# Kernel tuning notes

Measured on AMD Instinct MI355X. Metric: run time of the kernel, lower is better.

The kernel has to match this reference:

```python
import jax, jax.numpy as jnp
import numpy as np

K_TOP = 8
TEMP = 1.0
GUMBEL_EPS = 1e-20
GEN_EPS = 1e-7
NEG_INF = -1e9


def _genconv(xn, src, dst, e, We, be, W1, b1, W2, b2):
    """GENConv: edge-proj, m=relu(x_src+e)+eps, per-dst softmax aggregation (t=1),
    residual add, then 2-layer MLP."""
    N = xn.shape[0]
    ep = e @ We + be                         # [E, C]
    m = jax.nn.relu(xn[src] + ep) + GEN_EPS  # [E, C]
    mx = jax.ops.segment_max(m, dst, num_segments=N)
    mx = jnp.where(jnp.isfinite(mx), mx, 0.0)
    w = jnp.exp(m - mx[dst])
    den = jax.ops.segment_sum(w, dst, num_segments=N)
    agg = jax.ops.segment_sum(w * m, dst, num_segments=N) / jnp.where(den > 0, den, 1.0)
    out = agg + xn
    return jax.nn.relu(out @ W1 + b1) @ W2 + b2


def setup_inputs() -> dict:
    key = jax.random.key(0)
    ks = jax.random.split(key, 16)
    N, E, D, ED = 1024, 16384, 128, 16
    H1, H2, OUT = 64, 64, 40
    s = 0.02
    return {
        "x": jax.random.normal(ks[0], (N, D), jnp.float32),
        "edge_attr": jax.random.normal(ks[1], (E, ED), jnp.float32),
        "gumbel_u": jax.random.uniform(ks[2], (N, N), jnp.float32),
        "mlp_w": jax.random.normal(ks[3], (ED + 2 * D, 1), jnp.float32) * s,
        "mlp_b": jnp.zeros((1,), jnp.float32),
        "c1_we": jax.random.normal(ks[4], (ED, D), jnp.float32) * s,
        "c1_be": jnp.zeros((D,), jnp.float32),
        "c1_w1": jax.random.normal(ks[5], (D, 2 * D), jnp.float32) * s,
        "c1_b1": jnp.zeros((2 * D,), jnp.float32),
        "c1_w2": jax.random.normal(ks[6], (2 * D, H1), jnp.float32) * s,
        "c1_b2": jnp.zeros((H1,), jnp.float32),
        "c2_we": jax.random.normal(ks[7], (ED, H1), jnp.float32) * s,
        "c2_be": jnp.zeros((H1,), jnp.float32),
        "c2_w1": jax.random.normal(ks[8], (H1, 2 * H1), jnp.float32) * s,
        "c2_b1": jnp.zeros((2 * H1,), jnp.float32),
        "c2_w2": jax.random.normal(ks[9], (2 * H1, H2), jnp.float32) * s,
        "c2_b2": jnp.zeros((H2,), jnp.float32),
        "fc_w": jax.random.normal(ks[10], (H2, OUT), jnp.float32) * s,
        "fc_b": jnp.zeros((OUT,), jnp.float32),
        "num_nodes": N,
        "edge_index": jax.random.randint(ks[11], (2, E), 0, N),
        "node_mask": jnp.ones((N,), jnp.int32),
    }


def reference(x, edge_attr, gumbel_u, mlp_w, mlp_b,
              c1_we, c1_be, c1_w1, c1_b1, c1_w2, c1_b2,
              c2_we, c2_be, c2_w1, c2_b1, c2_w2, c2_b2,
              fc_w, fc_b, num_nodes, edge_index, node_mask):
    N, D = x.shape
    src, dst = edge_index[0], edge_index[1]

    # dense adjacency (duplicate edges sum, only used as a zero/nonzero mask)
    adj = jnp.zeros((N, N), x.dtype).at[src, dst].add(1.0)

    # Edge-score MLP on concat([x_u, x_v*mask, edge_attr_dense]) decomposed
    # linearly (same math as scoring the dense [N,N,2D+ED] feature tensor).
    w_node, w_nb, w_e = mlp_w[:D], mlp_w[D:2 * D], mlp_w[2 * D:]
    s_edge = jnp.zeros((N, N), x.dtype).at[src, dst].set((edge_attr @ w_e)[:, 0])
    score = (x @ w_node) + (x @ w_nb).T * (adj > 0) + s_edge + mlp_b[0]
    score = jnp.where(adj == 0, NEG_INF, score)

    z = jax.nn.softmax(score, axis=-1)
    g = -jnp.log(-jnp.log(gumbel_u + GUMBEL_EPS) + GUMBEL_EPS)
    z = jax.nn.softmax((z + g) / TEMP, axis=-1)

    # top-k edge sampling; softmax output is strictly positive so valid_mask
    # (z>0) is always all-True and shapes stay static at N*k edges.
    _, topi = jax.lax.top_k(z, K_TOP)                       # [N, k]
    new_src = jnp.repeat(jnp.arange(N), K_TOP)
    new_dst = topi.reshape(-1)

    # match each new edge against old edge list (argmax of boolean equality,
    # unmatched edges fall back to index 0 exactly as torch argmax does)
    eq = (edge_index[0][None, :] == new_src[:, None]) & \
         (edge_index[1][None, :] == new_dst[:, None])       # [N*k, E]
    new_attr = edge_attr[jnp.argmax(eq, axis=-1)]

    h = _genconv(x, new_src, new_dst, new_attr, c1_we, c1_be, c1_w1, c1_b1, c1_w2, c1_b2)
    h = jax.nn.relu(h)
    h = _genconv(h, new_src, new_dst, new_attr, c2_we, c2_be, c2_w1, c2_b1, c2_w2, c2_b2)
    h = jax.nn.relu(h)
    out = h @ fc_w + fc_b
    # node_mask is all ones, so x[node_mask != 0] == identity; masked write
    # keeps static shapes under jit.
    return jnp.where((node_mask != 0)[:, None], out, 0.0)
```

## Files before the change

kernel.cpp:

```cpp
#include <hip/hip_runtime.h>
#include <cfloat>

#define NN   1024
#define NE   16384
#define D0   128
#define EDIM 16
#define NH1  64
#define NOUT 40
#define KTOP 8
#define NEGINF (-1000000000.0f)
#define MAXDEG 64
#define PMAX   64

#define OFF_EM  0u
#define OFF_ND  32768u
#define OFF_H   65536u

__device__ __forceinline__ void amx(float& v, int& j, float ov, int oj) {
    if (ov > v || (ov == v && oj < j)) { v = ov; j = oj; }
}

__global__ __launch_bounds__(256) void topk_kernel(
    const float* __restrict__ x, const float* __restrict__ ea,
    const float* __restrict__ u, const float* __restrict__ mlp_w,
    const float* __restrict__ mlp_b, const int* __restrict__ ei,
    int* __restrict__ nd, int* __restrict__ em)
{
    __shared__ int idmx[4 * NN];
    __shared__ int idmn[4 * NN];
    __shared__ int plj[4 * PMAX];
    __shared__ int ple[4 * PMAX];
    __shared__ int np[4];
    const int t = threadIdx.x, lane = t & 63, w = t >> 6;
    const int r0 = blockIdx.x * 4;

    #pragma unroll
    for (int q = 0; q < 16; q++) { idmx[t + q * 256] = -1; idmn[t + q * 256] = 0x7FFFFFFF; }
    if (t < 4) np[t] = 0;
    __syncthreads();

    const int4* src4 = (const int4*)ei;
    #pragma unroll
    for (int q = 0; q < 16; q++) {
        int idx4 = t + q * 256;
        int4 v = src4[idx4];
        int e0 = idx4 * 4;
        #pragma unroll
        for (int c = 0; c < 4; c++) {
            int s = (c == 0) ? v.x : (c == 1) ? v.y : (c == 2) ? v.z : v.w;
            unsigned rr = (unsigned)(s - r0);
            if (rr < 4u) {
                int e = e0 + c;
                int d = ei[NE + e];
                atomicMax(&idmx[rr * NN + d], e);
                atomicMin(&idmn[rr * NN + d], e);
            }
        }
    }
    __syncthreads();

    #pragma unroll
    for (int q = 0; q < 16; q++) {
        int idx = t + q * 256;
        int e = idmx[idx];
        if (e >= 0) {
            int row = idx >> 10;
            int p = atomicAdd(&np[row], 1);
            if (p < PMAX) { plj[row * PMAX + p] = idx & 1023; ple[row * PMAX + p] = e; }
        }
    }
    __syncthreads();

    const int r = r0 + w;

    float part = x[r * D0 + lane] * mlp_w[lane] + x[r * D0 + 64 + lane] * mlp_w[64 + lane];
    for (int s2 = 32; s2; s2 >>= 1) part += __shfl_down(part, s2);
    const float arb = __shfl(part, 0) + mlp_b[0];

    float val[16];
    #pragma unroll
    for (int q = 0; q < 16; q++) val[q] = NEGINF;

    const int npw = min(np[w], PMAX);
    for (int p = 0; p < npw; p++) {
        int j = plj[w * PMAX + p], e = ple[w * PMAX + p];
        float pp = x[j * D0 + lane] * mlp_w[128 + lane]
                 + x[j * D0 + 64 + lane] * mlp_w[192 + lane];
        if (lane < 16) pp += ea[e * EDIM + lane] * mlp_w[256 + lane];
        for (int s2 = 32; s2; s2 >>= 1) pp += __shfl_down(pp, s2);
        float sc = __shfl(pp, 0) + arb;
        #pragma unroll
        for (int q = 0; q < 16; q++)
            if (q == (j >> 6) && lane == (j & 63)) val[q] = sc;
    }

    float lm = NEGINF;
    #pragma unroll
    for (int q = 0; q < 16; q++) lm = fmaxf(lm, val[q]);
    for (int s2 = 32; s2; s2 >>= 1) lm = fmaxf(lm, __shfl_down(lm, s2));
    const float rowmax = __shfl(lm, 0);
    const bool noedge = (rowmax == NEGINF);

    float ls = 0.f;
    #pragma unroll
    for (int q = 0; q < 16; q++) {
        float ev = noedge ? 1.0f : ((val[q] == NEGINF) ? 0.0f : expf(val[q] - rowmax));
        val[q] = ev; ls += ev;
    }
    for (int s2 = 32; s2; s2 >>= 1) ls += __shfl_down(ls, s2);
    const float rsum = __shfl(ls, 0);

    const float* ur = u + r * NN;
    #pragma unroll
    for (int q = 0; q < 16; q++) {
        float uu = ur[q * 64 + lane];
        float g = -logf(-logf(uu + 1e-20f) + 1e-20f);
        val[q] = val[q] / rsum + g;
    }

    for (int sel = 0; sel < KTOP; sel++) {
        float bv = -FLT_MAX; int bj = NN;
        #pragma unroll
        for (int q = 0; q < 16; q++) amx(bv, bj, val[q], q * 64 + lane);
        for (int s2 = 32; s2; s2 >>= 1) {
            float ov = __shfl_down(bv, s2); int oj = __shfl_down(bj, s2);
            amx(bv, bj, ov, oj);
        }
        int wj = __shfl(bj, 0);
        if (lane == 0) {
            int mn = idmn[w * NN + wj];
            em[r * KTOP + sel] = (mn == 0x7FFFFFFF) ? 0 : mn;
            nd[r * KTOP + sel] = wj;
        }
        #pragma unroll
        for (int q = 0; q < 16; q++)
            if (q == (wj >> 6) && lane == (wj & 63)) val[q] = -FLT_MAX;
    }
}

__global__ __launch_bounds__(256) void genconv1_kernel(
    const float* __restrict__ x, const float* __restrict__ ea,
    const float* __restrict__ we_g, const float* __restrict__ be,
    const float* __restrict__ w1, const float* __restrict__ b1,
    const float* __restrict__ w2, const float* __restrict__ b2,
    const int* __restrict__ nd, const int* __restrict__ em,
    float* __restrict__ h)
{
    __shared__ int   slots[2][MAXDEG];
    __shared__ float eatt[2][MAXDEG * EDIM];
    __shared__ float arow[2][D0];
    __shared__ float t1s[2][2 * D0];
    __shared__ int   cnts[2];
    const int t = threadIdx.x, sub = t >> 7, d = t & 127;
    const int r0 = blockIdx.x * 2;
    const int r = r0 + sub;
    if (t < 2) cnts[t] = 0;
    __syncthreads();

    const int4* nd4 = (const int4*)nd;
    #pragma unroll
    for (int q = 0; q < 8; q++) {
        int idx4 = t + q * 256;
        int4 v = nd4[idx4];
        int n0 = idx4 * 4;
        #pragma unroll
        for (int c = 0; c < 4; c++) {
            int dj = (c == 0) ? v.x : (c == 1) ? v.y : (c == 2) ? v.z : v.w;
            unsigned rr = (unsigned)(dj - r0);
            if (rr < 2u) {
                int p = atomicAdd(&cnts[rr], 1);
                if (p < MAXDEG) slots[rr][p] = n0 + c;
            }
        }
    }
    __syncthreads();
    const int cnt = min(cnts[sub], MAXDEG);
    if (d == 0) {
        for (int p = 1; p < cnt; p++) {
            int v = slots[sub][p]; int q = p - 1;
            while (q >= 0 && slots[sub][q] > v) { slots[sub][q + 1] = slots[sub][q]; q--; }
            slots[sub][q + 1] = v;
        }
    }
    __syncthreads();
    for (int q = d; q < cnt * EDIM; q += 128)
        eatt[sub][q] = ea[em[slots[sub][q >> 4]] * EDIM + (q & 15)];
    __syncthreads();

    float wed[EDIM];
    #pragma unroll
    for (int k = 0; k < EDIM; k++) wed[k] = we_g[k * D0 + d];
    const float bed = be[d];

    float mxv = -FLT_MAX;
    for (int idx = 0; idx < cnt; idx++) {
        int src = slots[sub][idx] >> 3;
        float ep = bed;
        #pragma unroll
        for (int k = 0; k < EDIM; k++) ep += eatt[sub][idx * EDIM + k] * wed[k];
        float m = fmaxf(x[src * D0 + d] + ep, 0.f) + 1e-7f;
        mxv = fmaxf(mxv, m);
    }
    float den = 0.f, num = 0.f;
    for (int idx = 0; idx < cnt; idx++) {
        int src = slots[sub][idx] >> 3;
        float ep = bed;
        #pragma unroll
        for (int k = 0; k < EDIM; k++) ep += eatt[sub][idx * EDIM + k] * wed[k];
        float m = fmaxf(x[src * D0 + d] + ep, 0.f) + 1e-7f;
        float w = expf(m - mxv);
        den += w; num += w * m;
    }
    float agg = cnt ? num / (den > 0.f ? den : 1.f) : 0.f;
    arow[sub][d] = agg + x[r * D0 + d];
    __syncthreads();

    float acc0 = b1[d], acc1 = b1[d + D0];
    for (int k = 0; k < D0; k++) {
        float av = arow[sub][k];
        acc0 += av * w1[k * 2 * D0 + d];
        acc1 += av * w1[k * 2 * D0 + d + D0];
    }
    t1s[sub][d] = fmaxf(acc0, 0.f);
    t1s[sub][d + D0] = fmaxf(acc1, 0.f);
    __syncthreads();
    if (d < NH1) {
        float acc = b2[d];
        for (int k = 0; k < 2 * D0; k++) acc += t1s[sub][k] * w2[k * NH1 + d];
        h[r * NH1 + d] = fmaxf(acc, 0.f);
    }
}

__global__ __launch_bounds__(256) void genconv2_kernel(
    const float* __restrict__ h, const float* __restrict__ ea,
    const float* __restrict__ we_g, const float* __restrict__ be,
    const float* __restrict__ w1, const float* __restrict__ b1,
    const float* __restrict__ w2, const float* __restrict__ b2,
    const float* __restrict__ fcw, const float* __restrict__ fcb,
    const int* __restrict__ nd, const int* __restrict__ em,
    const int* __restrict__ mask, float* __restrict__ out)
{
    __shared__ int   slots[4][MAXDEG];
    __shared__ float eatt[4][MAXDEG * EDIM];
    __shared__ float arow[4][NH1];
    __shared__ float t2s[4][2 * NH1];
    __shared__ float h2s[4][NH1];
    __shared__ int   cnts[4];
    const int t = threadIdx.x, sub = t >> 6, d = t & 63;
    const int r0 = blockIdx.x * 4;
    const int r = r0 + sub;
    if (t < 4) cnts[t] = 0;
    __syncthreads();

    const int4* nd4 = (const int4*)nd;
    #pragma unroll
    for (int q = 0; q < 8; q++) {
        int idx4 = t + q * 256;
        int4 v = nd4[idx4];
        int n0 = idx4 * 4;
        #pragma unroll
        for (int c = 0; c < 4; c++) {
            int dj = (c == 0) ? v.x : (c == 1) ? v.y : (c == 2) ? v.z : v.w;
            unsigned rr = (unsigned)(dj - r0);
            if (rr < 4u) {
                int p = atomicAdd(&cnts[rr], 1);
                if (p < MAXDEG) slots[rr][p] = n0 + c;
            }
        }
    }
    __syncthreads();
    const int cnt = min(cnts[sub], MAXDEG);
    if (d == 0) {
        for (int p = 1; p < cnt; p++) {
            int v = slots[sub][p]; int q = p - 1;
            while (q >= 0 && slots[sub][q] > v) { slots[sub][q + 1] = slots[sub][q]; q--; }
            slots[sub][q + 1] = v;
        }
    }
    __syncthreads();
    for (int q = d; q < cnt * EDIM; q += 64)
        eatt[sub][q] = ea[em[slots[sub][q >> 4]] * EDIM + (q & 15)];
    __syncthreads();

    float wed[EDIM];
    #pragma unroll
    for (int k = 0; k < EDIM; k++) wed[k] = we_g[k * NH1 + d];
    const float bed = be[d];

    float mxv = -FLT_MAX;
    for (int idx = 0; idx < cnt; idx++) {
        int src = slots[sub][idx] >> 3;
        float ep = bed;
        #pragma unroll
        for (int k = 0; k < EDIM; k++) ep += eatt[sub][idx * EDIM + k] * wed[k];
        float m = fmaxf(h[src * NH1 + d] + ep, 0.f) + 1e-7f;
        mxv = fmaxf(mxv, m);
    }
    float den = 0.f, num = 0.f;
    for (int idx = 0; idx < cnt; idx++) {
        int src = slots[sub][idx] >> 3;
        float ep = bed;
        #pragma unroll
        for (int k = 0; k < EDIM; k++) ep += eatt[sub][idx * EDIM + k] * wed[k];
        float m = fmaxf(h[src * NH1 + d] + ep, 0.f) + 1e-7f;
        float w = expf(m - mxv);
        den += w; num += w * m;
    }
    float agg = cnt ? num / (den > 0.f ? den : 1.f) : 0.f;
    arow[sub][d] = agg + h[r * NH1 + d];
    __syncthreads();

    {
        float acc_a = b1[d], acc_b = b1[d + NH1];
        for (int k = 0; k < NH1; k++) {
            float av = arow[sub][k];
            acc_a += av * w1[k * 2 * NH1 + d];
            acc_b += av * w1[k * 2 * NH1 + d + NH1];
        }
        t2s[sub][d] = fmaxf(acc_a, 0.f);
        t2s[sub][d + NH1] = fmaxf(acc_b, 0.f);
    }
    __syncthreads();
    {
        float acc = b2[d];
        for (int k = 0; k < 2 * NH1; k++) acc += t2s[sub][k] * w2[k * NH1 + d];
        h2s[sub][d] = fmaxf(acc, 0.f);
    }
    __syncthreads();
    if (d < NOUT) {
        float acc = fcb[d];
        for (int k = 0; k < NH1; k++) acc += h2s[sub][k] * fcw[k * NOUT + d];
        out[r * NOUT + d] = (mask[r] != 0) ? acc : 0.f;
    }
}

extern "C" void kernel_launch(void* const* d_in, const int* in_sizes, int n_in,
                              void* d_out, int out_size, void* d_ws, size_t ws_size,
                              hipStream_t stream) {
    const float* x      = (const float*)d_in[0];
    const float* ea     = (const float*)d_in[1];
    const float* u      = (const float*)d_in[2];
    const float* mlp_w  = (const float*)d_in[3];
    const float* mlp_b  = (const float*)d_in[4];
    const float* c1_we  = (const float*)d_in[5];
    const float* c1_be  = (const float*)d_in[6];
    const float* c1_w1  = (const float*)d_in[7];
    const float* c1_b1  = (const float*)d_in[8];
    const float* c1_w2  = (const float*)d_in[9];
    const float* c1_b2  = (const float*)d_in[10];
    const float* c2_we  = (const float*)d_in[11];
    const float* c2_be  = (const float*)d_in[12];
    const float* c2_w1  = (const float*)d_in[13];
    const float* c2_b1  = (const float*)d_in[14];
    const float* c2_w2  = (const float*)d_in[15];
    const float* c2_b2  = (const float*)d_in[16];
    const float* fc_w   = (const float*)d_in[17];
    const float* fc_b   = (const float*)d_in[18];
    const int*   ei     = (const int*)d_in[20];
    const int*   mask   = (const int*)d_in[21];

    char* ws = (char*)d_ws;
    int*   em = (int*)(ws + OFF_EM);
    int*   nd = (int*)(ws + OFF_ND);
    float* h  = (float*)(ws + OFF_H);
    float* out = (float*)d_out;

    topk_kernel<<<NN / 4, 256, 0, stream>>>(x, ea, u, mlp_w, mlp_b, ei, nd, em);
    genconv1_kernel<<<NN / 2, 256, 0, stream>>>(x, ea, c1_we, c1_be, c1_w1, c1_b1, c1_w2, c1_b2,
                                                nd, em, h);
    genconv2_kernel<<<NN / 4, 256, 0, stream>>>(h, ea, c2_we, c2_be, c2_w1, c2_b1, c2_w2, c2_b2,
                                                fc_w, fc_b, nd, em, mask, out);
}
```

Before: 180.4 us.

## Assign one top-k row per block and split the row across waves

The top-k kernel now handles a single row per 256-thread block instead of four rows per block. The four waves each own a quarter of the columns, reduce max and sum through shared memory, and pick local top-8 candidates, which wave 0 merges. This increases block count and parallelism and cuts per-lane register arrays and shared memory. In exchange, every block rescans the whole edge list, quadrupling total edge-index reads, and extra block-wide barriers are added.

New measurement: 162.0 us. 10.2% less time.

```diff
diff --git a/kernel.cpp b/kernel.cpp
--- a/kernel.cpp
+++ b/kernel.cpp
@@ -26,93 +26,92 @@
     const float* __restrict__ mlp_b, const int* __restrict__ ei,
     int* __restrict__ nd, int* __restrict__ em)
 {
-    __shared__ int idmx[4 * NN];
-    __shared__ int idmn[4 * NN];
-    __shared__ int plj[4 * PMAX];
-    __shared__ int ple[4 * PMAX];
-    __shared__ int np[4];
-    const int t = threadIdx.x, lane = t & 63, w = t >> 6;
-    const int r0 = blockIdx.x * 4;
-
-    #pragma unroll
-    for (int q = 0; q < 16; q++) { idmx[t + q * 256] = -1; idmn[t + q * 256] = 0x7FFFFFFF; }
-    if (t < 4) np[t] = 0;
-    __syncthreads();
-
-    const int4* src4 = (const int4*)ei;
+    __shared__ int   idmx[NN];
+    __shared__ int   idmn[NN];
+    __shared__ float sv[NN];
+    __shared__ int   plj[PMAX];
+    __shared__ int   ple[PMAX];
+    __shared__ int   np;
+    __shared__ float wred[8];
+    __shared__ float candv[32];
+    __shared__ int   candj[32];
+    const int i = blockIdx.x, t = threadIdx.x;
+    const int lane = t & 63, w = t >> 6;
+
+    #pragma unroll
+    for (int q = 0; q < 4; q++) {
+        int j = t + q * 256;
+        idmx[j] = -1; idmn[j] = 0x7FFFFFFF; sv[j] = NEGINF;
+    }
+    if (t == 0) np = 0;
+    __syncthreads();
+
+    const int4* s4 = (const int4*)ei;
     #pragma unroll
     for (int q = 0; q < 16; q++) {
         int idx4 = t + q * 256;
-        int4 v = src4[idx4];
+        int4 sv4 = s4[idx4];
         int e0 = idx4 * 4;
-        #pragma unroll
-        for (int c = 0; c < 4; c++) {
-            int s = (c == 0) ? v.x : (c == 1) ? v.y : (c == 2) ? v.z : v.w;
-            unsigned rr = (unsigned)(s - r0);
-            if (rr < 4u) {
-                int e = e0 + c;
-                int d = ei[NE + e];
-                atomicMax(&idmx[rr * NN + d], e);
-                atomicMin(&idmn[rr * NN + d], e);
-            }
-        }
-    }
-    __syncthreads();
-
-    #pragma unroll
-    for (int q = 0; q < 16; q++) {
-        int idx = t + q * 256;
-        int e = idmx[idx];
+        if (sv4.x == i) { int dj = ei[NE + e0 + 0]; atomicMax(&idmx[dj], e0 + 0); atomicMin(&idmn[dj], e0 + 0); }
+        if (sv4.y == i) { int dj = ei[NE + e0 + 1]; atomicMax(&idmx[dj], e0 + 1); atomicMin(&idmn[dj], e0 + 1); }
+        if (sv4.z == i) { int dj = ei[NE + e0 + 2]; atomicMax(&idmx[dj], e0 + 2); atomicMin(&idmn[dj], e0 + 2); }
+        if (sv4.w == i) { int dj = ei[NE + e0 + 3]; atomicMax(&idmx[dj], e0 + 3); atomicMin(&idmn[dj], e0 + 3); }
+    }
+    __syncthreads();
+
+    #pragma unroll
+    for (int q = 0; q < 4; q++) {
+        int j = t + q * 256;
+        int e = idmx[j];
         if (e >= 0) {
-            int row = idx >> 10;
-            int p = atomicAdd(&np[row], 1);
-            if (p < PMAX) { plj[row * PMAX + p] = idx & 1023; ple[row * PMAX + p] = e; }
-        }
-    }
-    __syncthreads();
-
-    const int r = r0 + w;
-
-    float part = x[r * D0 + lane] * mlp_w[lane] + x[r * D0 + 64 + lane] * mlp_w[64 + lane];
+            int p = atomicAdd(&np, 1);
+            if (p < PMAX) { plj[p] = j; ple[p] = e; }
+        }
+    }
+    __syncthreads();
+
+    float part = x[i * D0 + lane] * mlp_w[lane] + x[i * D0 + 64 + lane] * mlp_w[64 + lane];
     for (int s2 = 32; s2; s2 >>= 1) part += __shfl_down(part, s2);
     const float arb = __shfl(part, 0) + mlp_b[0];
 
-    float val[16];
-    #pragma unroll
-    for (int q = 0; q < 16; q++) val[q] = NEGINF;
-
-    const int npw = min(np[w], PMAX);
-    for (int p = 0; p < npw; p++) {
-        int j = plj[w * PMAX + p], e = ple[w * PMAX + p];
+    const int npc = min(np, PMAX);
+    for (int p = w; p < npc; p += 4) {
+        int j = plj[p], e = ple[p];
         float pp = x[j * D0 + lane] * mlp_w[128 + lane]
                  + x[j * D0 + 64 + lane] * mlp_w[192 + lane];
-        if (lane < 16) pp += ea[e * EDIM + lane] * mlp_w[256 + lane];
+        if (lane < 16) pp += ea[e * EDIM + lane] * mlp_w[2 * D0 + lane];
         for (int s2 = 32; s2; s2 >>= 1) pp += __shfl_down(pp, s2);
-        float sc = __shfl(pp, 0) + arb;
-        #pragma unroll
-        for (int q = 0; q < 16; q++)
-            if (q == (j >> 6) && lane == (j & 63)) val[q] = sc;
-    }
-
+        if (lane == 0) sv[j] = pp + arb;
+    }
+    __syncthreads();
+
+    float val[4];
     float lm = NEGINF;
     #pragma unroll
-    for (int q = 0; q < 16; q++) lm = fmaxf(lm, val[q]);
+    for (int q = 0; q < 4; q++) {
+        val[q] = sv[w * 256 + q * 64 + lane];
+        lm = fmaxf(lm, val[q]);
+    }
     for (int s2 = 32; s2; s2 >>= 1) lm = fmaxf(lm, __shfl_down(lm, s2));
-    const float rowmax = __shfl(lm, 0);
+    if (lane == 0) wred[w] = lm;
+    __syncthreads();
+    const float rowmax = fmaxf(fmaxf(wred[0], wred[1]), fmaxf(wred[2], wred[3]));
     const bool noedge = (rowmax == NEGINF);
 
     float ls = 0.f;
     #pragma unroll
-    for (int q = 0; q < 16; q++) {
+    for (int q = 0; q < 4; q++) {
         float ev = noedge ? 1.0f : ((val[q] == NEGINF) ? 0.0f : expf(val[q] - rowmax));
         val[q] = ev; ls += ev;
     }
     for (int s2 = 32; s2; s2 >>= 1) ls += __shfl_down(ls, s2);
-    const float rsum = __shfl(ls, 0);
-
-    const float* ur = u + r * NN;
-    #pragma unroll
-    for (int q = 0; q < 16; q++) {
+    if (lane == 0) wred[4 + w] = ls;
+    __syncthreads();
+    const float rsum = wred[4] + wred[5] + wred[6] + wred[7];
+
+    const float* ur = u + i * NN + w * 256;
+    #pragma unroll
+    for (int q = 0; q < 4; q++) {
         float uu = ur[q * 64 + lane];
         float g = -logf(-logf(uu + 1e-20f) + 1e-20f);
         val[q] = val[q] / rsum + g;
@@ -121,20 +120,36 @@
     for (int sel = 0; sel < KTOP; sel++) {
         float bv = -FLT_MAX; int bj = NN;
         #pragma unroll
-        for (int q = 0; q < 16; q++) amx(bv, bj, val[q], q * 64 + lane);
+        for (int q = 0; q < 4; q++) amx(bv, bj, val[q], w * 256 + q * 64 + lane);
         for (int s2 = 32; s2; s2 >>= 1) {
             float ov = __shfl_down(bv, s2); int oj = __shfl_down(bj, s2);
             amx(bv, bj, ov, oj);
         }
         int wj = __shfl(bj, 0);
-        if (lane == 0) {
-            int mn = idmn[w * NN + wj];
-            em[r * KTOP + sel] = (mn == 0x7FFFFFFF) ? 0 : mn;
-            nd[r * KTOP + sel] = wj;
-        }
-        #pragma unroll
-        for (int q = 0; q < 16; q++)
-            if (q == (wj >> 6) && lane == (wj & 63)) val[q] = -FLT_MAX;
+        if (lane == 0) { candv[w * KTOP + sel] = bv; candj[w * KTOP + sel] = bj; }
+        #pragma unroll
+        for (int q = 0; q < 4; q++)
+            if (w * 256 + q * 64 + lane == wj) val[q] = -FLT_MAX;
+    }
+    __syncthreads();
+
+    if (w == 0) {
+        float mv = (lane < 32) ? candv[lane] : -FLT_MAX;
+        int   mj = (lane < 32) ? candj[lane] : NN;
+        for (int sel = 0; sel < KTOP; sel++) {
+            float bv = mv; int bj = mj;
+            for (int s2 = 32; s2; s2 >>= 1) {
+                float ov = __shfl_down(bv, s2); int oj = __shfl_down(bj, s2);
+                amx(bv, bj, ov, oj);
+            }
+            int wj = __shfl(bj, 0);
+            if (lane == 0) {
+                int mn = idmn[wj];
+                em[i * KTOP + sel] = (mn == 0x7FFFFFFF) ? 0 : mn;
+                nd[i * KTOP + sel] = wj;
+            }
+            if (mj == wj) mv = -FLT_MAX;
+        }
     }
 }
 
@@ -365,7 +380,7 @@
     float* h  = (float*)(ws + OFF_H);
     float* out = (float*)d_out;
 
-    topk_kernel<<<NN / 4, 256, 0, stream>>>(x, ea, u, mlp_w, mlp_b, ei, nd, em);
+    topk_kernel<<<NN, 256, 0, stream>>>(x, ea, u, mlp_w, mlp_b, ei, nd, em);
     genconv1_kernel<<<NN / 2, 256, 0, stream>>>(x, ea, c1_we, c1_be, c1_w1, c1_b1, c1_w2, c1_b2,
                                                 nd, em, h);
     genconv2_kernel<<<NN / 4, 256, 0, stream>>>(h, ea, c2_we, c2_be, c2_w1, c2_b1, c2_w2, c2_b2,
```
